# Kernel optimization log

Measured on AMD Instinct MI355X. Metric: run time of the kernel, lower is better.

Reference implementation:

```python
import jax, jax.numpy as jnp
import numpy as np
import itertools

# ---- model dimensions ----
NELEC = 10   # total electrons
NSPIN = 2    # spin_split = 2 -> equal split (5, 5)
NPER = 5     # electrons per spin block
D = 3        # spatial dimension
NION = 2     # number of ions (diatomic)
DP = 32      # backflow output feature dim d'
NDENSE = 64  # ndense_resnet


def _perms_and_signs(n):
    perms = np.array(list(itertools.permutations(range(n))), dtype=np.int32)
    signs = np.empty(len(perms), dtype=np.float32)
    for i, p in enumerate(perms):
        inv = sum(1 for a in range(n) for b in range(a + 1, n) if p[a] > p[b])
        signs[i] = -1.0 if inv % 2 else 1.0
    return jnp.asarray(perms), jnp.asarray(signs)

# constant permutation indices/signs (closed over; not differentiated)
PERMS, SIGNS = _perms_and_signs(NPER)  # (120, 5), (120,)


def setup_inputs() -> dict:
    key = jax.random.key(0)
    ks = jax.random.split(key, 8)
    B = 2048
    feat = NION * D + NION  # backflow input features per electron: r_ei flat + |r_ei|
    nin = NPER * DP         # flattened spin-block input to each ResNet
    return {
        "elec_pos": jax.random.normal(ks[0], (B, NELEC, D), jnp.float32),
        "ion_pos": jax.random.normal(ks[1], (NION, D), jnp.float32) * 2.0,
        "bf_w": jax.random.normal(ks[2], (feat, DP), jnp.float32) / np.sqrt(feat),
        "bf_b": jnp.zeros((DP,), jnp.float32),
        "w0": jax.random.normal(ks[3], (NSPIN, nin, NDENSE), jnp.float32) / np.sqrt(nin),
        "b0": jnp.zeros((NSPIN, NDENSE), jnp.float32),
        "w1": jax.random.normal(ks[4], (NSPIN, NDENSE, NDENSE), jnp.float32) / np.sqrt(NDENSE),
        "b1": jnp.zeros((NSPIN, NDENSE), jnp.float32),
        "w2": jax.random.normal(ks[5], (NSPIN, NDENSE, 1), jnp.float32) / np.sqrt(NDENSE),
        "b2": jnp.zeros((NSPIN, 1), jnp.float32),
        "jastrow_kernel": jnp.ones((NION,), jnp.float32),
    }


def _spin_antisym(block, W0, B0, W1, B1, W2, B2):
    # block: (B, NPER, DP) one spin block of the 1e stream
    B = block.shape[0]
    xp = block[:, PERMS, :]                  # (B, nperm, NPER, DP) all permutations
    xp = xp.reshape(B, PERMS.shape[0], NPER * DP)
    # SimpleResNet: dense->act, residual middle layer, final linear to 1
    h = jnp.tanh(xp @ W0 + B0)
    h = jnp.tanh(h @ W1 + B1) + h            # residual (shapes match)
    out = (h @ W2 + B2)[..., 0]              # (B, nperm)
    return jnp.sum(out * SIGNS, axis=-1)     # signed perm-sum -> (B,)


def reference(elec_pos, ion_pos, bf_w, bf_b, w0, b0, w1, b1, w2, b2, jastrow_kernel):
    B = elec_pos.shape[0]
    # backflow: r_ei features -> dense -> tanh
    r_ei = elec_pos[..., :, None, :] - ion_pos          # (B, nelec, nion, d)
    r_norm = jnp.linalg.norm(r_ei, axis=-1)             # (B, nelec, nion)
    feats = jnp.concatenate([r_ei.reshape(B, NELEC, NION * D), r_norm], axis=-1)
    stream_1e = jnp.tanh(feats @ bf_w + bf_b)           # (B, nelec, DP)
    # split into equal spin blocks (spin_split=2)
    blocks = jnp.stack(jnp.split(stream_1e, NSPIN, axis=-2), axis=0)  # (NSPIN, B, NPER, DP)
    per_spin = jax.vmap(_spin_antisym)(blocks, w0, b0, w1, b1, w2, b2)  # (NSPIN, B)
    antisymmetric_part = jnp.log(jnp.abs(jnp.prod(per_spin, axis=0)))   # (B,)
    # isotropic atomic exponential decay jastrow (log domain)
    jastrow_part = -jnp.sum(jastrow_kernel * r_norm, axis=(-1, -2))     # (B,)
    return antisymmetric_part + jastrow_part
```

## Files before the change

kernel.cpp:

```cpp
#include <hip/hip_runtime.h>
#include <math.h>

#define NELEC 10
#define NSPIN 2
#define NPER 5
#define DIM 3
#define NION 2
#define DP 32
#define NDENSE 64
#define NPERM 120
#define RS 324
#define HTS 124
#define KQ 16

#define POOL_WORDS (160 + NPER * RS + KQ * HTS)

typedef float v2f __attribute__((ext_vector_type(2)));
typedef float v4f __attribute__((ext_vector_type(4)));

#define PK_FMA_LO(acc, hp, wp) \
    asm("v_pk_fma_f32 %0, %1, %2, %0 op_sel_hi:[1,0,1]" : "+v"(acc) : "v"(hp), "v"(wp))
#define PK_FMA_HI(acc, hp, wp) \
    asm("v_pk_fma_f32 %0, %1, %2, %0 op_sel:[0,1,0] op_sel_hi:[1,1,1]" : "+v"(acc) : "v"(hp), "v"(wp))

__device__ __forceinline__ float fast_tanh(float x) {
    float e = __expf(2.0f * x);
    return 1.0f - 2.0f * __builtin_amdgcn_rcpf(e + 1.0f);
}

__device__ __forceinline__ unsigned pick_remove(unsigned& el, int d) {
    unsigned v = (el >> (4 * d)) & 0xFu;
    unsigned low = el & ((1u << (4 * d)) - 1u);
    el = low | ((el >> (4 * (d + 1))) << (4 * d));
    return v;
}

__global__ __launch_bounds__(256, 1) __attribute__((amdgpu_num_vgpr(128)))
void antisym_fused(
    const float* __restrict__ elec_pos, const float* __restrict__ ion_pos,
    const float* __restrict__ bf_w, const float* __restrict__ bf_b,
    const float* __restrict__ w0, const float* __restrict__ b0,
    const float* __restrict__ w1, const float* __restrict__ b1,
    const float* __restrict__ w2, const float* __restrict__ jk,
    float* __restrict__ out, int B)
{
    const int b = blockIdx.x;
    const int t = threadIdx.x;
    const int s = t >> 7;
    const int ts = t & 127;
    const int wave = (t >> 6) & 1;
    const int lane = t & 63;

    __shared__ __align__(16) float pool[NSPIN][POOL_WORDS];
    __shared__ double red_h[NSPIN][2];
    __shared__ double red_j[NSPIN][2];
    __shared__ float jterm[2 * NELEC];

    float* s1e = pool[s];
    #define GROW(j)   (pool[s] + 160 + (j) * RS)
    #define HTQROW(k) (pool[s] + 160 + NPER * RS + (k) * HTS)

    const float* ep = elec_pos + (b * NELEC + s * NPER) * DIM;
    const float i0x = ion_pos[0], i0y = ion_pos[1], i0z = ion_pos[2];
    const float i1x = ion_pos[3], i1y = ion_pos[4], i1z = ion_pos[5];
    for (int idx = ts; idx < NPER * DP; idx += 128) {
        int j = idx >> 5, c = idx & 31;
        float ex = ep[j * 3 + 0], ey = ep[j * 3 + 1], ez = ep[j * 3 + 2];
        float dx0 = ex - i0x, dy0 = ey - i0y, dz0 = ez - i0z;
        float dx1 = ex - i1x, dy1 = ey - i1y, dz1 = ez - i1z;
        float n0 = sqrtf(dx0 * dx0 + dy0 * dy0 + dz0 * dz0);
        float n1 = sqrtf(dx1 * dx1 + dy1 * dy1 + dz1 * dz1);
        float acc = bf_b[c];
        acc += dx0 * bf_w[0 * DP + c];
        acc += dy0 * bf_w[1 * DP + c];
        acc += dz0 * bf_w[2 * DP + c];
        acc += dx1 * bf_w[3 * DP + c];
        acc += dy1 * bf_w[4 * DP + c];
        acc += dz1 * bf_w[5 * DP + c];
        acc += n0 * bf_w[6 * DP + c];
        acc += n1 * bf_w[7 * DP + c];
        s1e[idx] = fast_tanh(acc);
    }
    if (t < 2 * NELEC) {
        int e = t >> 1, ion = t & 1;
        const float* epb = elec_pos + b * NELEC * DIM;
        float ex = epb[e * 3 + 0], ey = epb[e * 3 + 1], ez = epb[e * 3 + 2];
        float ix = ion_pos[ion * 3 + 0], iy = ion_pos[ion * 3 + 1], iz = ion_pos[ion * 3 + 2];
        float dx = ex - ix, dy = ey - iy, dz = ez - iz;
        jterm[t] = jk[ion] * sqrtf(dx * dx + dy * dy + dz * dz);
    }
    __syncthreads();

    const float* w0s = w0 + s * (NPER * DP) * NDENSE;
    #pragma unroll
    for (int m = 0; m < 3; m++) {
        const int i = wave + 2 * m;
        if (i < NPER) {
            float wcol[DP];
            #pragma unroll
            for (int k = 0; k < DP; k++) wcol[k] = w0s[(i * DP + k) * NDENSE + lane];
            #pragma unroll
            for (int j = 0; j < NPER; j++) {
                float acc = 0.f;
                #pragma unroll
                for (int q = 0; q < 8; q++) {
                    float4 sv = *(const float4*)(s1e + j * DP + q * 4);
                    acc += sv.x * wcol[q * 4 + 0];
                    acc += sv.y * wcol[q * 4 + 1];
                    acc += sv.z * wcol[q * 4 + 2];
                    acc += sv.w * wcol[q * 4 + 3];
                }
                GROW(j)[i * NDENSE + lane] = acc;
            }
        }
    }
    __syncthreads();

    const float* b0s = b0 + s * NDENSE;
    const float* w2s = w2 + s * NDENSE;
    const float* b1s = b1 + s * NDENSE;
    const float* w1s = w1 + s * NDENSE * NDENSE;

    const int pid = wave * 60 + lane;
    float sign = 0.f;
    int p0 = 0, p1 = 0, p2 = 0, p3 = 0, p4 = 0;
    if (lane < 60) {
        int p = pid;
        unsigned el = 0x43210u;
        int d0 = p / 24; p -= d0 * 24;
        int d1 = p / 6;  p -= d1 * 6;
        int d2 = p / 2;  p -= d2 * 2;
        int d3 = p;
        p0 = pick_remove(el, d0);
        p1 = pick_remove(el, d1);
        p2 = pick_remove(el, d2);
        p3 = pick_remove(el, d3);
        p4 = el & 0xF;
        sign = ((d0 + d1 + d2 + d3) & 1) ? -1.f : 1.f;
    }
    const float* g0 = GROW(p0) + 0 * NDENSE;
    const float* g1 = GROW(p1) + 1 * NDENSE;
    const float* g2 = GROW(p2) + 2 * NDENSE;
    const float* g3 = GROW(p3) + 3 * NDENSE;
    const float* g4 = GROW(p4) + 4 * NDENSE;

    const int pg = lane >> 3, jg = lane & 7;
    const int pb = wave ? (56 + 8 * pg) : (8 * pg);
    const float* wgp = w1s + 8 * jg;

    v2f vp[4][8];
    #pragma unroll
    for (int ip = 0; ip < 4; ip++)
        #pragma unroll
        for (int r = 0; r < 8; r++) vp[ip][r] = (v2f)(0.f);

    float hdot = 0.f;

    for (int qq = 0; qq < 4; qq++) {
        #pragma unroll
        for (int c = 0; c < 4; c++) {
            const int cc = qq * 4 + c;
            float4 a = *(const float4*)(b0s + cc * 4);
            float4 q;
            q = *(const float4*)(g0 + cc * 4); a.x += q.x; a.y += q.y; a.z += q.z; a.w += q.w;
            q = *(const float4*)(g1 + cc * 4); a.x += q.x; a.y += q.y; a.z += q.z; a.w += q.w;
            q = *(const float4*)(g2 + cc * 4); a.x += q.x; a.y += q.y; a.z += q.z; a.w += q.w;
            q = *(const float4*)(g3 + cc * 4); a.x += q.x; a.y += q.y; a.z += q.z; a.w += q.w;
            q = *(const float4*)(g4 + cc * 4); a.x += q.x; a.y += q.y; a.z += q.z; a.w += q.w;
            float t0 = fast_tanh(a.x), t1 = fast_tanh(a.y), t2 = fast_tanh(a.z), t3 = fast_tanh(a.w);
            if (lane < 60) {
                HTQROW(c * 4 + 0)[pid] = t0;
                HTQROW(c * 4 + 1)[pid] = t1;
                HTQROW(c * 4 + 2)[pid] = t2;
                HTQROW(c * 4 + 3)[pid] = t3;
            }
            hdot += t0 * w2s[cc * 4 + 0] + t1 * w2s[cc * 4 + 1]
                  + t2 * w2s[cc * 4 + 2] + t3 * w2s[cc * 4 + 3];
        }
        __syncthreads();

        #pragma unroll 4
        for (int kk = 0; kk < KQ; kk++) {
            const v4f ha = *(const v4f*)(&HTQROW(kk)[pb]);
            const v4f hb = *(const v4f*)(&HTQROW(kk)[pb + 4]);
            const v4f wa = *(const v4f*)(wgp + (qq * KQ + kk) * NDENSE);
            const v4f wb = *(const v4f*)(wgp + (qq * KQ + kk) * NDENSE + 4);
            v2f hp[4] = {ha.xy, ha.zw, hb.xy, hb.zw};
            v2f wp[4] = {wa.xy, wa.zw, wb.xy, wb.zw};
            #pragma unroll
            for (int ip = 0; ip < 4; ip++) {
                PK_FMA_LO(vp[ip][0], hp[ip], wp[0]);
                PK_FMA_HI(vp[ip][1], hp[ip], wp[0]);
                PK_FMA_LO(vp[ip][2], hp[ip], wp[1]);
                PK_FMA_HI(vp[ip][3], hp[ip], wp[1]);
                PK_FMA_LO(vp[ip][4], hp[ip], wp[2]);
                PK_FMA_HI(vp[ip][5], hp[ip], wp[2]);
                PK_FMA_LO(vp[ip][6], hp[ip], wp[3]);
                PK_FMA_HI(vp[ip][7], hp[ip], wp[3]);
            }
        }
        __syncthreads();
    }

    double dvh = (double)(sign * hdot);
    #pragma unroll
    for (int off = 32; off > 0; off >>= 1) dvh += __shfl_down(dvh, off, 64);
    if (lane == 0) red_h[s][wave] = dvh;

    float4 b1a = *(const float4*)(b1s + 8 * jg);
    float4 b1b = *(const float4*)(b1s + 8 * jg + 4);
    float4 w2a = *(const float4*)(w2s + 8 * jg);
    float4 w2b = *(const float4*)(w2s + 8 * jg + 4);
    const float b1v[8] = {b1a.x, b1a.y, b1a.z, b1a.w, b1b.x, b1b.y, b1b.z, b1b.w};
    const float w2v[8] = {w2a.x, w2a.y, w2a.z, w2a.w, w2b.x, w2b.y, w2b.z, w2b.w};

    float lanesum = 0.f;
    #pragma unroll
    for (int i = 0; i < 8; i++) {
        int p = pb + i;
        int d0 = p / 24;  int r0 = p - 24 * d0;
        int d1 = r0 / 6;  int r1 = r0 - 6 * d1;
        int d2 = r1 >> 1; int d3 = r1 & 1;
        float sgn = ((d0 + d1 + d2 + d3) & 1) ? -1.f : 1.f;
        if (wave == 1 && pg == 0) sgn = 0.f;
        float si = 0.f;
        #pragma unroll
        for (int r = 0; r < 8; r++) {
            float vir = (i & 1) ? vp[i >> 1][r].y : vp[i >> 1][r].x;
            si = fmaf(fast_tanh(vir + b1v[r]), w2v[r], si);
        }
        lanesum = fmaf(sgn, si, lanesum);
    }

    double dvj = (double)lanesum;
    #pragma unroll
    for (int off = 32; off > 0; off >>= 1) dvj += __shfl_down(dvj, off, 64);
    if (lane == 0) red_j[s][wave] = dvj;
    __syncthreads();

    if (t == 0) {
        float ps0 = (float)((red_h[0][0] + red_h[0][1]) + (red_j[0][0] + red_j[0][1]));
        float ps1 = (float)((red_h[1][0] + red_h[1][1]) + (red_j[1][0] + red_j[1][1]));
        float jas = 0.f;
        #pragma unroll
        for (int i = 0; i < 2 * NELEC; i++) jas += jterm[i];
        out[b] = logf(fabsf(ps0 * ps1)) - jas;
    }
}

extern "C" void kernel_launch(void* const* d_in, const int* in_sizes, int n_in,
                              void* d_out, int out_size, void* d_ws, size_t ws_size,
                              hipStream_t stream) {
    const float* elec_pos = (const float*)d_in[0];
    const float* ion_pos  = (const float*)d_in[1];
    const float* bf_w     = (const float*)d_in[2];
    const float* bf_b     = (const float*)d_in[3];
    const float* w0       = (const float*)d_in[4];
    const float* b0       = (const float*)d_in[5];
    const float* w1       = (const float*)d_in[6];
    const float* b1       = (const float*)d_in[7];
    const float* w2       = (const float*)d_in[8];
    const float* jk       = (const float*)d_in[10];
    float* out = (float*)d_out;

    const int B = in_sizes[0] / (NELEC * DIM);

    hipLaunchKernelGGL(antisym_fused,
                       dim3(B), dim3(256), 0, stream,
                       elec_pos, ion_pos, bf_w, bf_b, w0, b0, w1, b1, w2, jk, out, B);
}
```

Measured before the change: 162.1 us.

## Keep per-permutation hidden vector in registers and stage W1 in LDS

The kernel restructures the second dense layer so that each lane owns one permutation. The lane keeps its 64-wide tanh activation in registers and reads W1 rows from LDS as broadcast loads. W1 is copied once from global memory into LDS, which removes the transposed h-tile staging and the four rounds of block barriers inside the layer loop. Each lane now does the full 64x64 matvec, so the FMA work per lane rises, and the W1 loads are uniform LDS broadcasts. Lanes 60-63 in each wave still compute but are masked out through a zero sign, and LDS use per block grows to hold W1.

```diff
diff --git a/kernel.cpp b/kernel.cpp
--- a/kernel.cpp
+++ b/kernel.cpp
@@ -10,18 +10,17 @@
 #define NDENSE 64
 #define NPERM 120
 #define RS 324
-#define HTS 124
-#define KQ 16
-
-#define POOL_WORDS (160 + NPER * RS + KQ * HTS)
+#define W1OFF (160 + NPER * RS)
+#define POOL_WORDS (W1OFF + NDENSE * NDENSE)
+
 
 typedef float v2f __attribute__((ext_vector_type(2)));
 typedef float v4f __attribute__((ext_vector_type(4)));
 
-#define PK_FMA_LO(acc, hp, wp) \
-    asm("v_pk_fma_f32 %0, %1, %2, %0 op_sel_hi:[1,0,1]" : "+v"(acc) : "v"(hp), "v"(wp))
-#define PK_FMA_HI(acc, hp, wp) \
-    asm("v_pk_fma_f32 %0, %1, %2, %0 op_sel:[0,1,0] op_sel_hi:[1,1,1]" : "+v"(acc) : "v"(hp), "v"(wp))
+#define PK_FMA_BL(acc, hp, wp) \
+    asm("v_pk_fma_f32 %0, %1, %2, %0 op_sel_hi:[0,1,1]" : "+v"(acc) : "v"(hp), "v"(wp))
+#define PK_FMA_BH(acc, hp, wp) \
+    asm("v_pk_fma_f32 %0, %1, %2, %0 op_sel:[1,0,0] op_sel_hi:[1,1,1]" : "+v"(acc) : "v"(hp), "v"(wp))
 
 __device__ __forceinline__ float fast_tanh(float x) {
     float e = __expf(2.0f * x);
@@ -52,13 +51,12 @@
     const int lane = t & 63;
 
     __shared__ __align__(16) float pool[NSPIN][POOL_WORDS];
-    __shared__ double red_h[NSPIN][2];
-    __shared__ double red_j[NSPIN][2];
+    __shared__ double red[NSPIN][2];
     __shared__ float jterm[2 * NELEC];
 
     float* s1e = pool[s];
-    #define GROW(j)   (pool[s] + 160 + (j) * RS)
-    #define HTQROW(k) (pool[s] + 160 + NPER * RS + (k) * HTS)
+    #define GROW(j) (pool[s] + 160 + (j) * RS)
+    float* w1L = pool[s] + W1OFF;
 
     const float* ep = elec_pos + (b * NELEC + s * NPER) * DIM;
     const float i0x = ion_pos[0], i0y = ion_pos[1], i0z = ion_pos[2];
@@ -80,6 +78,11 @@
         acc += n0 * bf_w[6 * DP + c];
         acc += n1 * bf_w[7 * DP + c];
         s1e[idx] = fast_tanh(acc);
+    }
+    {
+        const float* w1g = w1 + s * NDENSE * NDENSE;
+        for (int idx = ts; idx < (NDENSE * NDENSE) / 4; idx += 128)
+            ((float4*)w1L)[idx] = ((const float4*)w1g)[idx];
     }
     if (t < 2 * NELEC) {
         int e = t >> 1, ion = t & 1;
@@ -119,7 +122,6 @@
     const float* b0s = b0 + s * NDENSE;
     const float* w2s = w2 + s * NDENSE;
     const float* b1s = b1 + s * NDENSE;
-    const float* w1s = w1 + s * NDENSE * NDENSE;
 
     const int pid = wave * 60 + lane;
     float sign = 0.f;
@@ -144,103 +146,70 @@
     const float* g3 = GROW(p3) + 3 * NDENSE;
     const float* g4 = GROW(p4) + 4 * NDENSE;
 
-    const int pg = lane >> 3, jg = lane & 7;
-    const int pb = wave ? (56 + 8 * pg) : (8 * pg);
-    const float* wgp = w1s + 8 * jg;
-
-    v2f vp[4][8];
+    v2f hp2[NDENSE / 2];
+    float hdot = 0.f;
     #pragma unroll
-    for (int ip = 0; ip < 4; ip++)
-        #pragma unroll
-        for (int r = 0; r < 8; r++) vp[ip][r] = (v2f)(0.f);
-
-    float hdot = 0.f;
-
-    for (int qq = 0; qq < 4; qq++) {
-        #pragma unroll
-        for (int c = 0; c < 4; c++) {
-            const int cc = qq * 4 + c;
-            float4 a = *(const float4*)(b0s + cc * 4);
-            float4 q;
-            q = *(const float4*)(g0 + cc * 4); a.x += q.x; a.y += q.y; a.z += q.z; a.w += q.w;
-            q = *(const float4*)(g1 + cc * 4); a.x += q.x; a.y += q.y; a.z += q.z; a.w += q.w;
-            q = *(const float4*)(g2 + cc * 4); a.x += q.x; a.y += q.y; a.z += q.z; a.w += q.w;
-            q = *(const float4*)(g3 + cc * 4); a.x += q.x; a.y += q.y; a.z += q.z; a.w += q.w;
-            q = *(const float4*)(g4 + cc * 4); a.x += q.x; a.y += q.y; a.z += q.z; a.w += q.w;
-            float t0 = fast_tanh(a.x), t1 = fast_tanh(a.y), t2 = fast_tanh(a.z), t3 = fast_tanh(a.w);
-            if (lane < 60) {
-                HTQROW(c * 4 + 0)[pid] = t0;
-                HTQROW(c * 4 + 1)[pid] = t1;
-                HTQROW(c * 4 + 2)[pid] = t2;
-                HTQROW(c * 4 + 3)[pid] = t3;
-            }
-            hdot += t0 * w2s[cc * 4 + 0] + t1 * w2s[cc * 4 + 1]
-                  + t2 * w2s[cc * 4 + 2] + t3 * w2s[cc * 4 + 3];
+    for (int cc = 0; cc < NDENSE / 4; cc++) {
+        float4 a = *(const float4*)(b0s + cc * 4);
+        float4 q;
+        q = *(const float4*)(g0 + cc * 4); a.x += q.x; a.y += q.y; a.z += q.z; a.w += q.w;
+        q = *(const float4*)(g1 + cc * 4); a.x += q.x; a.y += q.y; a.z += q.z; a.w += q.w;
+        q = *(const float4*)(g2 + cc * 4); a.x += q.x; a.y += q.y; a.z += q.z; a.w += q.w;
+        q = *(const float4*)(g3 + cc * 4); a.x += q.x; a.y += q.y; a.z += q.z; a.w += q.w;
+        q = *(const float4*)(g4 + cc * 4); a.x += q.x; a.y += q.y; a.z += q.z; a.w += q.w;
+        float t0 = fast_tanh(a.x), t1 = fast_tanh(a.y), t2 = fast_tanh(a.z), t3 = fast_tanh(a.w);
+        v2f u; u.x = t0; u.y = t1; hp2[2 * cc] = u;
+        v2f v; v.x = t2; v.y = t3; hp2[2 * cc + 1] = v;
+        hdot += t0 * w2s[cc * 4 + 0] + t1 * w2s[cc * 4 + 1]
+              + t2 * w2s[cc * 4 + 2] + t3 * w2s[cc * 4 + 3];
+    }
+
+    double jsumd = 0.0;
+    #pragma unroll 1
+    for (int q = 0; q < 4; ++q) {
+        v2f acc[8];
+        #pragma unroll
+        for (int r = 0; r < 8; r++) acc[r] = (v2f)(0.f);
+        const float* wq = w1L + q * 16;
+        #pragma unroll
+        for (int m = 0; m < 32; m++) {
+            const float* r0 = wq + (2 * m) * NDENSE;
+            const float* r1 = wq + (2 * m + 1) * NDENSE;
+            const v2f hp = hp2[m];
+            v4f a0 = *(const v4f*)(r0),     a1 = *(const v4f*)(r0 + 4);
+            v4f e0 = *(const v4f*)(r1),     e1 = *(const v4f*)(r1 + 4);
+            PK_FMA_BL(acc[0], hp, a0.xy);  PK_FMA_BL(acc[1], hp, a0.zw);
+            PK_FMA_BL(acc[2], hp, a1.xy);  PK_FMA_BL(acc[3], hp, a1.zw);
+            PK_FMA_BH(acc[0], hp, e0.xy);  PK_FMA_BH(acc[1], hp, e0.zw);
+            PK_FMA_BH(acc[2], hp, e1.xy);  PK_FMA_BH(acc[3], hp, e1.zw);
+            v4f c0 = *(const v4f*)(r0 + 8), c1 = *(const v4f*)(r0 + 12);
+            v4f f0 = *(const v4f*)(r1 + 8), f1 = *(const v4f*)(r1 + 12);
+            PK_FMA_BL(acc[4], hp, c0.xy);  PK_FMA_BL(acc[5], hp, c0.zw);
+            PK_FMA_BL(acc[6], hp, c1.xy);  PK_FMA_BL(acc[7], hp, c1.zw);
+            PK_FMA_BH(acc[4], hp, f0.xy);  PK_FMA_BH(acc[5], hp, f0.zw);
+            PK_FMA_BH(acc[6], hp, f1.xy);  PK_FMA_BH(acc[7], hp, f1.zw);
         }
-        __syncthreads();
-
-        #pragma unroll 4
-        for (int kk = 0; kk < KQ; kk++) {
-            const v4f ha = *(const v4f*)(&HTQROW(kk)[pb]);
-            const v4f hb = *(const v4f*)(&HTQROW(kk)[pb + 4]);
-            const v4f wa = *(const v4f*)(wgp + (qq * KQ + kk) * NDENSE);
-            const v4f wb = *(const v4f*)(wgp + (qq * KQ + kk) * NDENSE + 4);
-            v2f hp[4] = {ha.xy, ha.zw, hb.xy, hb.zw};
-            v2f wp[4] = {wa.xy, wa.zw, wb.xy, wb.zw};
-            #pragma unroll
-            for (int ip = 0; ip < 4; ip++) {
-                PK_FMA_LO(vp[ip][0], hp[ip], wp[0]);
-                PK_FMA_HI(vp[ip][1], hp[ip], wp[0]);
-                PK_FMA_LO(vp[ip][2], hp[ip], wp[1]);
-                PK_FMA_HI(vp[ip][3], hp[ip], wp[1]);
-                PK_FMA_LO(vp[ip][4], hp[ip], wp[2]);
-                PK_FMA_HI(vp[ip][5], hp[ip], wp[2]);
-                PK_FMA_LO(vp[ip][6], hp[ip], wp[3]);
-                PK_FMA_HI(vp[ip][7], hp[ip], wp[3]);
-            }
+        float si0 = 0.f, si1 = 0.f;
+        #pragma unroll
+        for (int r = 0; r < 8; r++) {
+            float v0 = (r & 1) ? acc[r >> 1].y : acc[r >> 1].x;
+            si0 = fmaf(fast_tanh(v0 + b1s[q * 16 + r]), w2s[q * 16 + r], si0);
+            float v1 = (r & 1) ? acc[4 + (r >> 1)].y : acc[4 + (r >> 1)].x;
+            si1 = fmaf(fast_tanh(v1 + b1s[q * 16 + 8 + r]), w2s[q * 16 + 8 + r], si1);
         }
-        __syncthreads();
-    }
-
-    double dvh = (double)(sign * hdot);
+        jsumd += (double)si0;
+        jsumd += (double)si1;
+    }
+
+    double dv = (double)(sign * hdot) + (double)sign * jsumd;
     #pragma unroll
-    for (int off = 32; off > 0; off >>= 1) dvh += __shfl_down(dvh, off, 64);
-    if (lane == 0) red_h[s][wave] = dvh;
-
-    float4 b1a = *(const float4*)(b1s + 8 * jg);
-    float4 b1b = *(const float4*)(b1s + 8 * jg + 4);
-    float4 w2a = *(const float4*)(w2s + 8 * jg);
-    float4 w2b = *(const float4*)(w2s + 8 * jg + 4);
-    const float b1v[8] = {b1a.x, b1a.y, b1a.z, b1a.w, b1b.x, b1b.y, b1b.z, b1b.w};
-    const float w2v[8] = {w2a.x, w2a.y, w2a.z, w2a.w, w2b.x, w2b.y, w2b.z, w2b.w};
-
-    float lanesum = 0.f;
-    #pragma unroll
-    for (int i = 0; i < 8; i++) {
-        int p = pb + i;
-        int d0 = p / 24;  int r0 = p - 24 * d0;
-        int d1 = r0 / 6;  int r1 = r0 - 6 * d1;
-        int d2 = r1 >> 1; int d3 = r1 & 1;
-        float sgn = ((d0 + d1 + d2 + d3) & 1) ? -1.f : 1.f;
-        if (wave == 1 && pg == 0) sgn = 0.f;
-        float si = 0.f;
-        #pragma unroll
-        for (int r = 0; r < 8; r++) {
-            float vir = (i & 1) ? vp[i >> 1][r].y : vp[i >> 1][r].x;
-            si = fmaf(fast_tanh(vir + b1v[r]), w2v[r], si);
-        }
-        lanesum = fmaf(sgn, si, lanesum);
-    }
-
-    double dvj = (double)lanesum;
-    #pragma unroll
-    for (int off = 32; off > 0; off >>= 1) dvj += __shfl_down(dvj, off, 64);
-    if (lane == 0) red_j[s][wave] = dvj;
+    for (int off = 32; off > 0; off >>= 1) dv += __shfl_down(dv, off, 64);
+    if (lane == 0) red[s][wave] = dv;
     __syncthreads();
 
     if (t == 0) {
-        float ps0 = (float)((red_h[0][0] + red_h[0][1]) + (red_j[0][0] + red_j[0][1]));
-        float ps1 = (float)((red_h[1][0] + red_h[1][1]) + (red_j[1][0] + red_j[1][1]));
+        float ps0 = (float)(red[0][0] + red[0][1]);
+        float ps1 = (float)(red[1][0] + red[1][1]);
         float jas = 0.f;
         #pragma unroll
         for (int i = 0; i < 2 * NELEC; i++) jas += jterm[i];
```

New measurement: 173.1 us. 1.07x slower.
